# Performance work log

Hardware: AMD Instinct MI355X
Metric: run time of the kernel (lower is better)

Reference implementation:

```python
import jax, jax.numpy as jnp
import numpy as np

BN_EPS = 1e-5
VQ_TEMP = 0.1

B, K, D_AUDIO, D_TEXT, VOCAB = 256, 8, 768, 512, 49408


def setup_inputs() -> dict:
    key = jax.random.key(0)
    k1, k2, k3, k4, k5 = jax.random.split(key, 5)
    return {
        "audio_kw": jax.random.normal(k1, (B, K, D_AUDIO), dtype=jnp.float32),
        "W_proj": jax.random.normal(k2, (D_AUDIO, D_TEXT), dtype=jnp.float32) * 0.02,
        "b_proj": jnp.zeros((D_TEXT,), dtype=jnp.float32),
        "bn_gamma": jax.random.uniform(k3, (D_TEXT,), dtype=jnp.float32, minval=0.5, maxval=1.5),
        "bn_beta": jax.random.normal(k4, (D_TEXT,), dtype=jnp.float32) * 0.01,
        "emb": jax.random.normal(k5, (VOCAB, D_TEXT), dtype=jnp.float32) * 0.02,
    }


def reference(audio_kw, W_proj, b_proj, bn_gamma, bn_beta, emb):
    # keyword projection: [B,K,Da] @ [Da,Dt] -> [B,K,Dt]
    proj = jnp.einsum("bkd,de->bke", audio_kw, W_proj) + b_proj
    # Kw_BatchNorm: batchnorm over (batch, keyword) per text feature, affine
    mean = jnp.mean(proj, axis=(0, 1))
    var = jnp.var(proj, axis=(0, 1))
    bn = (proj - mean) * jax.lax.rsqrt(var + BN_EPS) * bn_gamma + bn_beta
    # cosine similarity against full vocab table (one fused normalize+GEMM,
    # equivalent to the per-keyword F.cosine_similarity loop in the original)
    bn_n = bn / jnp.linalg.norm(bn, axis=-1, keepdims=True)
    emb_n = emb / jnp.linalg.norm(emb, axis=-1, keepdims=True)
    cos_score = jnp.einsum("bke,ve->bkv", bn_n, emb_n)  # [B,K,V]
    # VQ: temperature softmax over the vocab, then soft lookup
    subword_prob = jax.nn.softmax(cos_score / VQ_TEMP, axis=-1)
    vq_keywords = jnp.einsum("bkv,ve->bke", subword_prob, emb)  # [B,K,Dt]
    return vq_keywords
```

## Files before the change

### kernel.cpp

```cpp
#include <hip/hip_runtime.h>
#include <stdint.h>

typedef unsigned short u16;
typedef _Float16 f16;
typedef __attribute__((ext_vector_type(8))) _Float16 f16x8;
typedef __attribute__((ext_vector_type(4))) float f32x4;

#define DA 768
#define DT 512
#define NV 49408
#define MTOT 2048
#define NB_N 193
#define KS 16

__device__ __forceinline__ u16 f2h(float f) {
  return __builtin_bit_cast(u16, (f16)f);
}

__device__ __forceinline__ void gload16(const void* g, void* l) {
  __builtin_amdgcn_global_load_lds((const __attribute__((address_space(1))) void*)g,
                                   (__attribute__((address_space(3))) void*)l,
                                   16, 0, 0);
}
#define SBAR()   __builtin_amdgcn_s_barrier()
#define SCHED0() __builtin_amdgcn_sched_barrier(0)
#define MFMA16(a, b, c) __builtin_amdgcn_mfma_f32_16x16x32_f16((a), (b), (c), 0, 0, 0)

__global__ __launch_bounds__(256) void k_a2h(const float* __restrict__ a,
                                             u16* __restrict__ ah) {
  int i = (blockIdx.x * 256 + threadIdx.x) * 8;
  float4 x = *(const float4*)&a[i];
  float4 y = *(const float4*)&a[i + 4];
  union { u16 u[8]; int4 q; } pk;
  pk.u[0] = f2h(x.x); pk.u[1] = f2h(x.y); pk.u[2] = f2h(x.z); pk.u[3] = f2h(x.w);
  pk.u[4] = f2h(y.x); pk.u[5] = f2h(y.y); pk.u[6] = f2h(y.z); pk.u[7] = f2h(y.w);
  *(int4*)&ah[i] = pk.q;
}

__global__ __launch_bounds__(256) void k_wT(const float* __restrict__ W,
                                            u16* __restrict__ WT) {
  __shared__ float tile[64][65];
  const int k0 = blockIdx.y * 64, n0 = blockIdx.x * 64;
  const int t = threadIdx.x;
  const int r = t >> 4, c4 = (t & 15) * 4;
#pragma unroll
  for (int i = 0; i < 4; ++i) {
    float4 x = *(const float4*)&W[(size_t)(k0 + r + i * 16) * DT + n0 + c4];
    tile[r + i * 16][c4 + 0] = x.x; tile[r + i * 16][c4 + 1] = x.y;
    tile[r + i * 16][c4 + 2] = x.z; tile[r + i * 16][c4 + 3] = x.w;
  }
  __syncthreads();
  const int nr = t >> 2, kc = (t & 3) * 16;
  union { u16 u[8]; int4 q; } p0, p1;
#pragma unroll
  for (int i = 0; i < 8; ++i) p0.u[i] = f2h(tile[kc + i][nr]);
#pragma unroll
  for (int i = 0; i < 8; ++i) p1.u[i] = f2h(tile[kc + 8 + i][nr]);
  u16* dst = WT + (size_t)(n0 + nr) * DA + k0 + kc;
  *(int4*)dst = p0.q;
  *(int4*)(dst + 8) = p1.q;
}

__global__ __launch_bounds__(256) void k_stats(const float* __restrict__ P,
                                               float* __restrict__ pstat) {
  const int t = threadIdx.x;
  const int r0 = blockIdx.x * 32;
  float s0 = 0, q0 = 0, s1 = 0, q1 = 0;
  for (int r = r0; r < r0 + 32; ++r) {
    float x0 = P[(size_t)r * DT + t];
    float x1 = P[(size_t)r * DT + t + 256];
    s0 += x0; q0 += x0 * x0; s1 += x1; q1 += x1 * x1;
  }
  float* d = pstat + (size_t)blockIdx.x * 1024;
  d[t] = s0; d[t + 256] = s1; d[512 + t] = q0; d[768 + t] = q1;
}

__global__ __launch_bounds__(256) void k_stats2(const float* __restrict__ pstat,
                                                float* __restrict__ stats) {
  int c = blockIdx.x * 256 + threadIdx.x;
  float s = 0.f;
  for (int b = 0; b < 64; ++b) s += pstat[(size_t)b * 1024 + c];
  stats[c] = s;
}

__global__ __launch_bounds__(64) void k_bnnorm(const float* __restrict__ P,
                                               const float* __restrict__ stats,
                                               const float* __restrict__ gamma,
                                               const float* __restrict__ beta,
                                               u16* __restrict__ bnn) {
  const int r = blockIdx.x, l = threadIdx.x;
  float v[8];
  float ss = 0.f;
#pragma unroll
  for (int i = 0; i < 8; ++i) {
    int c = l * 8 + i;
    float mean = stats[c] * (1.f / MTOT);
    float var = stats[DT + c] * (1.f / MTOT) - mean * mean;
    float is = rsqrtf(var + 1e-5f);
    float x = (P[(size_t)r * DT + c] - mean) * is * gamma[c] + beta[c];
    v[i] = x; ss += x * x;
  }
#pragma unroll
  for (int off = 32; off > 0; off >>= 1) ss += __shfl_xor(ss, off);
  float rn = rsqrtf(ss);
  union { u16 u[8]; int4 q; } pk;
#pragma unroll
  for (int i = 0; i < 8; ++i) pk.u[i] = f2h(v[i] * rn);
  *(int4*)&bnn[(size_t)r * DT + l * 8] = pk.q;
}

__global__ __launch_bounds__(256) void k_embprep2(const float* __restrict__ emb,
                                                  u16* __restrict__ embH,
                                                  u16* __restrict__ embT,
                                                  float* __restrict__ invn) {
  __shared__ float tile[64][65];
  const int v0 = blockIdx.x * 64;
  const int t = threadIdx.x;
  const int r = t >> 4, c4 = (t & 15) * 4;
  const int vr = t >> 2, hc = (t & 3) * 16;
  const int dr = t >> 2, vc = (t & 3) * 16;
  float ssq = 0.f;
  for (int d0 = 0; d0 < DT; d0 += 64) {
    __syncthreads();
#pragma unroll
    for (int i = 0; i < 4; ++i) {
      float4 x = *(const float4*)&emb[(size_t)(v0 + r + i * 16) * DT + d0 + c4];
      tile[r + i * 16][c4 + 0] = x.x; tile[r + i * 16][c4 + 1] = x.y;
      tile[r + i * 16][c4 + 2] = x.z; tile[r + i * 16][c4 + 3] = x.w;
    }
    __syncthreads();
    union { u16 u[8]; int4 q; } pa, pb;
#pragma unroll
    for (int i = 0; i < 8; ++i) { float f = tile[vr][hc + i];     pa.u[i] = f2h(f); ssq += f * f; }
#pragma unroll
    for (int i = 0; i < 8; ++i) { float f = tile[vr][hc + 8 + i]; pb.u[i] = f2h(f); ssq += f * f; }
    *(int4*)&embH[(size_t)(v0 + vr) * DT + d0 + hc] = pa.q;
    *(int4*)&embH[(size_t)(v0 + vr) * DT + d0 + hc + 8] = pb.q;
    union { u16 u[8]; int4 q; } p0, p1;
#pragma unroll
    for (int i = 0; i < 8; ++i) p0.u[i] = f2h(tile[vc + i][dr]);
#pragma unroll
    for (int i = 0; i < 8; ++i) p1.u[i] = f2h(tile[vc + 8 + i][dr]);
    u16* dst = embT + (size_t)(d0 + dr) * NV + v0 + vc;
    *(int4*)dst = p0.q;
    *(int4*)(dst + 8) = p1.q;
  }
  ssq += __shfl_xor(ssq, 1);
  ssq += __shfl_xor(ssq, 2);
  if ((t & 3) == 0) invn[v0 + vr] = rsqrtf(ssq) * 10.0f;
}

__device__ __forceinline__ void kloop256(const f16* __restrict__ A,
                                         const f16* __restrict__ B,
                                         int lda, int ldb, int NT,
                                         int m0, int n0, int tid,
                                         f16* ldsA, f16* ldsB,
                                         f32x4 (&acc)[4][4]) {
  const int l = tid & 63, lr = l & 15, lg = l >> 4;
  const int w = tid >> 6, wm = w >> 2, wn = w & 3;
  const int rA = tid >> 2, qA = tid & 3;
  const int qsA = qA ^ ((rA >> 1) & 3);
  const f16* gA = A + (size_t)(m0 + rA) * lda + qsA * 8;
  const f16* gB0;
  const f16* gB1;
  { int r = tid >> 2, q = tid & 3; int qs = q ^ ((r >> 1) & 3);
    gB0 = B + (size_t)(n0 + r) * ldb + qs * 8; }
  { int c = tid + 512; int r = c >> 2, q = c & 3; int qs = q ^ ((r >> 1) & 3);
    gB1 = B + (size_t)(n0 + r) * ldb + qs * 8; }
  auto STAGE = [&](int buf, int k0) {
    gload16(gA + k0, (void*)&ldsA[(size_t)buf * 4096 + (size_t)tid * 8]);
    gload16(gB0 + k0, (void*)&ldsB[(size_t)buf * 8192 + (size_t)tid * 8]);
    gload16(gB1 + k0, (void*)&ldsB[(size_t)buf * 8192 + (size_t)(tid + 512) * 8]);
  };
  const int gsw = lg ^ ((lr >> 1) & 3);

  STAGE(0, 0);
  STAGE(1, 32);
  asm volatile("s_waitcnt vmcnt(3)" ::: "memory"); SCHED0();
  SBAR(); SCHED0();
  int cur = 0;
  for (int it = 0; it < NT; ++it) {
    const f16* bufA = ldsA + cur * 4096;
    const f16* bufB = ldsB + cur * 8192;
    f16x8 af[4], bf[4];
#pragma unroll
    for (int i = 0; i < 4; ++i)
      af[i] = *(const f16x8*)&bufA[(wm * 64 + i * 16 + lr) * 32 + gsw * 8];
#pragma unroll
    for (int j = 0; j < 4; ++j)
      bf[j] = *(const f16x8*)&bufB[(wn * 64 + j * 16 + lr) * 32 + gsw * 8];
#pragma unroll
    for (int i = 0; i < 4; ++i)
#pragma unroll
      for (int j = 0; j < 4; ++j)
        acc[i][j] = MFMA16(af[i], bf[j], acc[i][j]);
    asm volatile("s_waitcnt lgkmcnt(0)" ::: "memory"); SCHED0();
    SBAR(); SCHED0();
    if (it + 2 < NT) {
      STAGE(cur, (it + 2) * 32);
      asm volatile("s_waitcnt vmcnt(3)" ::: "memory");
    } else {
      asm volatile("s_waitcnt vmcnt(0)" ::: "memory");
    }
    SCHED0();
    SBAR(); SCHED0();
    cur ^= 1;
  }
}

__global__ __launch_bounds__(512) void k_proj(const f16* __restrict__ A,
                                              const f16* __restrict__ Bt,
                                              const float* __restrict__ bias,
                                              float* __restrict__ P) {
  __shared__ f16 sm[24576];
  const int t = threadIdx.x;
  const int l = t & 63, lr = l & 15, lg = l >> 4;
  const int w = t >> 6, wm = w >> 2, wn = w & 3;
  const int m0 = blockIdx.x * 128;
  const int n0 = blockIdx.y * 256;

  f32x4 acc[4][4];
#pragma unroll
  for (int i = 0; i < 4; ++i)
#pragma unroll
    for (int j = 0; j < 4; ++j) acc[i][j] = (f32x4){0.f, 0.f, 0.f, 0.f};

  kloop256(A, Bt, DA, DA, DA / 32, m0, n0, t, sm, sm + 8192, acc);

#pragma unroll
  for (int j = 0; j < 4; ++j) {
    int col = n0 + wn * 64 + j * 16 + lr;
    float bj = bias[col];
#pragma unroll
    for (int i = 0; i < 4; ++i)
#pragma unroll
      for (int rg = 0; rg < 4; ++rg) {
        int row = m0 + wm * 64 + i * 16 + lg * 4 + rg;
        P[(size_t)row * DT + col] = acc[i][j][rg] + bj;
      }
  }
}

__global__ __launch_bounds__(512) void k_score(const f16* __restrict__ A,
                                               const f16* __restrict__ Bt,
                                               const float* __restrict__ invn,
                                               u16* __restrict__ E,
                                               float* __restrict__ lpart,
                                               int row0, int CH) {
  __shared__ f16 sm[24576];
  __shared__ float psum[512];
  const int t = threadIdx.x;
  const int l = t & 63, lr = l & 15, lg = l >> 4;
  const int w = t >> 6, wm = w >> 2, wn = w & 3;
  const int mB = CH >> 7;
  const int nwg = NB_N * mB;
  const int o = blockIdx.x + blockIdx.y * NB_N;
  const int v = (o & 7) * (nwg >> 3) + (o >> 3);
  const int nb = v / mB, by = v % mB;
  const int n0 = nb * 256;
  const int mloc = by * 128;
  const int m0 = row0 + mloc;

  f32x4 acc[4][4];
#pragma unroll
  for (int i = 0; i < 4; ++i)
#pragma unroll
    for (int j = 0; j < 4; ++j) acc[i][j] = (f32x4){0.f, 0.f, 0.f, 0.f};

  kloop256(A, Bt, DT, DT, DT / 32, m0, n0, t, sm, sm + 8192, acc);

  float inv_j[4];
#pragma unroll
  for (int j = 0; j < 4; ++j) inv_j[j] = invn[n0 + wn * 64 + j * 16 + lr];
  float rs[4][4] = {};
#pragma unroll
  for (int r2 = 0; r2 < 2; ++r2) {
    if (wm == r2) {
#pragma unroll
      for (int i = 0; i < 4; ++i)
#pragma unroll
        for (int j = 0; j < 4; ++j)
#pragma unroll
          for (int rg = 0; rg < 4; ++rg) {
            float e = __expf(acc[i][j][rg] * inv_j[j]);
            rs[i][rg] += e;
            int lrow = i * 16 + lg * 4 + rg;
            sm[lrow * 256 + wn * 64 + j * 16 + lr] = (f16)e;
          }
    }
    __syncthreads();
#pragma unroll
    for (int cc = 0; cc < 4; ++cc) {
      int chunk = t + cc * 512;
      int row = chunk >> 5, g = chunk & 31;
      *(int4*)&E[(size_t)(mloc + r2 * 64 + row) * NV + n0 + g * 8] =
          *(const int4*)&sm[chunk * 8];
    }
    __syncthreads();
  }
#pragma unroll
  for (int m = 1; m <= 8; m <<= 1)
#pragma unroll
    for (int i = 0; i < 4; ++i)
#pragma unroll
      for (int rg = 0; rg < 4; ++rg) rs[i][rg] += __shfl_xor(rs[i][rg], m);
  if (lr == 0) {
#pragma unroll
    for (int i = 0; i < 4; ++i)
#pragma unroll
      for (int rg = 0; rg < 4; ++rg)
        psum[(wm * 64 + i * 16 + lg * 4 + rg) * 4 + wn] = rs[i][rg];
  }
  __syncthreads();
  if (t < 128)
    lpart[(size_t)nb * CH + mloc + t] =
        psum[t * 4 + 0] + psum[t * 4 + 1] + psum[t * 4 + 2] + psum[t * 4 + 3];
}

__global__ __launch_bounds__(512) void k_pv(const f16* __restrict__ A,
                                            const f16* __restrict__ Bt,
                                            float* __restrict__ Op,
                                            int CH) {
  extern __shared__ char lds[];
  f16* ldsA = (f16*)lds;
  f16* ldsB = (f16*)(lds + 16384);
  const int t = threadIdx.x;
  const int l = t & 63, lr = l & 15, lg = l >> 4;
  const int w = t >> 6, wm = w >> 2, wn = w & 3;
  const int mB = CH >> 7;
  const int nwg = mB * KS;
  const int o = blockIdx.x;
  const int v = (o & 7) * (nwg >> 3) + (o >> 3);
  const int m = v % mB, z = v / mB;
  const int m0 = m * 128;
  const int g0 = z * 96 + (z < 8 ? z : 8);
  const int NT = 96 + (z < 8 ? 1 : 0);
  const size_t kb = (size_t)g0 * 32;

  const int rA = t >> 2, qA = t & 3;
  const int qsA = qA ^ ((rA >> 1) & 3);
  const f16* gA = A + (size_t)(m0 + rA) * NV + kb + qsA * 8;
  const f16* gB[4];
#pragma unroll
  for (int s = 0; s < 4; ++s) {
    int c = t + 512 * s;
    int r = c >> 2, q = c & 3;
    int qs = q ^ ((r >> 1) & 3);
    gB[s] = Bt + (size_t)r * NV + kb + qs * 8;
  }
  auto STAGE = [&](int buf, int kt) {
    int k0 = kt * 32;
    gload16(gA + k0, (void*)&ldsA[(size_t)buf * 4096 + (size_t)t * 8]);
    gload16(gB[0] + k0, (void*)&ldsB[(size_t)buf * 16384 + (size_t)t * 8]);
    gload16(gB[1] + k0, (void*)&ldsB[(size_t)buf * 16384 + (size_t)(t + 512) * 8]);
    gload16(gB[2] + k0, (void*)&ldsB[(size_t)buf * 16384 + (size_t)(t + 1024) * 8]);
    gload16(gB[3] + k0, (void*)&ldsB[(size_t)buf * 16384 + (size_t)(t + 1536) * 8]);
  };
  const int gsw = lg ^ ((lr >> 1) & 3);

  f32x4 acc[4][8];
#pragma unroll
  for (int i = 0; i < 4; ++i)
#pragma unroll
    for (int j = 0; j < 8; ++j) acc[i][j] = (f32x4){0.f, 0.f, 0.f, 0.f};

  STAGE(0, 0);
  STAGE(1, 1);
  asm volatile("s_waitcnt vmcnt(5)" ::: "memory"); SCHED0();
  SBAR(); SCHED0();
  int cur = 0;
  for (int it = 0; it < NT; ++it) {
    const f16* bufA = ldsA + cur * 4096;
    const f16* bufB = ldsB + cur * 16384;
    f16x8 af[4], bf[8];
#pragma unroll
    for (int i = 0; i < 4; ++i)
      af[i] = *(const f16x8*)&bufA[(wm * 64 + i * 16 + lr) * 32 + gsw * 8];
#pragma unroll
    for (int j = 0; j < 8; ++j)
      bf[j] = *(const f16x8*)&bufB[(wn * 128 + j * 16 + lr) * 32 + gsw * 8];
#pragma unroll
    for (int i = 0; i < 4; ++i)
#pragma unroll
      for (int j = 0; j < 8; ++j)
        acc[i][j] = MFMA16(af[i], bf[j], acc[i][j]);
    asm volatile("s_waitcnt lgkmcnt(0)" ::: "memory"); SCHED0();
    SBAR(); SCHED0();
    if (it + 2 < NT) {
      STAGE(cur, it + 2);
      asm volatile("s_waitcnt vmcnt(5)" ::: "memory");
    } else {
      asm volatile("s_waitcnt vmcnt(0)" ::: "memory");
    }
    SCHED0();
    SBAR(); SCHED0();
    cur ^= 1;
  }

#pragma unroll
  for (int i = 0; i < 4; ++i)
#pragma unroll
    for (int j = 0; j < 8; ++j)
#pragma unroll
      for (int rg = 0; rg < 4; ++rg) {
        int row = m0 + wm * 64 + i * 16 + lg * 4 + rg;
        int col = wn * 128 + j * 16 + lr;
        Op[((size_t)z * CH + row) * DT + col] = acc[i][j][rg];
      }
}

__global__ __launch_bounds__(256) void k_lred(const float* __restrict__ lp,
                                              float* __restrict__ lv, int CH) {
  int rb = blockIdx.x * 256 + threadIdx.x;
  float s = 0.f;
  for (int nb = 0; nb < NB_N; ++nb) s += lp[(size_t)nb * CH + rb];
  lv[rb] = s;
}

__global__ __launch_bounds__(256) void k_out(const float* __restrict__ Op,
                                             const float* __restrict__ lv,
                                             float* __restrict__ out,
                                             int row0, int CH) {
  int idx = blockIdx.x * 256 + threadIdx.x;
  int rb = idx >> 9, c = idx & 511;
  float s = 0.f;
#pragma unroll
  for (int zz = 0; zz < KS; ++zz) s += Op[((size_t)zz * CH + rb) * DT + c];
  out[(size_t)(row0 + rb) * DT + c] = s / lv[rb];
}

extern "C" void kernel_launch(void* const* d_in, const int* in_sizes, int n_in,
                              void* d_out, int out_size, void* d_ws, size_t ws_size,
                              hipStream_t stream) {
  const float* audio = (const float*)d_in[0];
  const float* W     = (const float*)d_in[1];
  const float* bias  = (const float*)d_in[2];
  const float* gamma = (const float*)d_in[3];
  const float* beta  = (const float*)d_in[4];
  const float* emb   = (const float*)d_in[5];
  float* out = (float*)d_out;

  char* ws = (char*)d_ws;
  size_t off = 0;
  auto alloc = [&](size_t bytes) {
    char* p = ws + off;
    off += (bytes + 255) & ~(size_t)255;
    return p;
  };
  float* proj   = (float*)alloc((size_t)MTOT * DT * 4);
  float* pstat  = (float*)alloc((size_t)64 * 1024 * 4);
  float* stats  = (float*)alloc((size_t)2 * DT * 4);
  u16*   bnnH   = (u16*)alloc((size_t)MTOT * DT * 2);
  u16*   embH   = (u16*)alloc((size_t)NV * DT * 2);
  u16*   embT   = (u16*)alloc((size_t)DT * NV * 2);
  float* invn   = (float*)alloc((size_t)NV * 4);
  u16*   audioH = (u16*)alloc((size_t)MTOT * DA * 2);
  u16*   WT     = (u16*)alloc((size_t)DT * DA * 2);
  size_t fixed_off = off;

  int CH = 2048;
  while (CH > 256) {
    size_t need = fixed_off;
    need += (((size_t)CH * NV * 2) + 255) & ~(size_t)255;
    need += (((size_t)NB_N * CH * 4) + 255) & ~(size_t)255;
    need += (((size_t)CH * 4) + 255) & ~(size_t)255;
    need += (((size_t)KS * CH * DT * 4) + 255) & ~(size_t)255;
    if (need <= ws_size) break;
    CH >>= 1;
  }
  u16*   E     = (u16*)alloc((size_t)CH * NV * 2);
  float* lpart = (float*)alloc((size_t)NB_N * CH * 4);
  float* lvec  = (float*)alloc((size_t)CH * 4);
  float* Op    = (float*)alloc((size_t)KS * CH * DT * 4);
  if (ws_size < off) return;

  hipFuncSetAttribute((const void*)k_pv,
                      hipFuncAttributeMaxDynamicSharedMemorySize, 81920);

  k_a2h<<<dim3(MTOT * DA / 2048), dim3(256), 0, stream>>>(audio, audioH);
  k_wT<<<dim3(DT / 64, DA / 64), dim3(256), 0, stream>>>(W, WT);
  k_proj<<<dim3(MTOT / 128, 2), dim3(512), 0, stream>>>(
      (const f16*)audioH, (const f16*)WT, bias, proj);
  k_stats<<<dim3(64), dim3(256), 0, stream>>>(proj, pstat);
  k_stats2<<<dim3(4), dim3(256), 0, stream>>>(pstat, stats);
  k_bnnorm<<<dim3(MTOT), dim3(64), 0, stream>>>(proj, stats, gamma, beta, bnnH);
  k_embprep2<<<dim3(NV / 64), dim3(256), 0, stream>>>(emb, embH, embT, invn);

  for (int row0 = 0; row0 < MTOT; row0 += CH) {
    k_score<<<dim3(NB_N, CH / 128), dim3(512), 0, stream>>>(
        (const f16*)bnnH, (const f16*)embH, invn, E, lpart, row0, CH);
    k_lred<<<dim3(CH / 256), dim3(256), 0, stream>>>(lpart, lvec, CH);
    k_pv<<<dim3((CH >> 7) * KS), dim3(512), 81920, stream>>>(
        (const f16*)E, (const f16*)embT, Op, CH);
    k_out<<<dim3(CH * 2), dim3(256), 0, stream>>>(Op, lvec, out, row0, CH);
  }
}
```

Baseline: 415.4 us.

## Enlarge score kernel tile to 256x256 with 1024 threads and inline K-loop

The score GEMM workgroup grows from a 128x256 to a 256x256 output tile using 16 waves (1024 threads). It uses a custom double-buffered global_load_lds K-loop with XOR-swizzled LDS and dynamic shared memory, and a remainder-aware XCD block remapping. The larger tile is meant to raise embedding-tile reuse and halve the number of workgroups. The cost is lower occupancy per CU, more LDS per block, and more complex indexing.

```diff
diff --git a/kernel.cpp b/kernel.cpp
--- a/kernel.cpp
+++ b/kernel.cpp
@@ -241,33 +241,81 @@
   }
 }
 
-__global__ __launch_bounds__(512) void k_score(const f16* __restrict__ A,
-                                               const f16* __restrict__ Bt,
-                                               const float* __restrict__ invn,
-                                               u16* __restrict__ E,
-                                               float* __restrict__ lpart,
-                                               int row0, int CH) {
-  __shared__ f16 sm[24576];
-  __shared__ float psum[512];
+__global__ __launch_bounds__(1024) void k_score(const f16* __restrict__ A,
+                                                const f16* __restrict__ Bt,
+                                                const float* __restrict__ invn,
+                                                u16* __restrict__ E,
+                                                float* __restrict__ lpart,
+                                                int row0, int CH) {
+  extern __shared__ char lds[];
+  f16* sm = (f16*)lds;
+  float* psum = (float*)(lds + 65536);
   const int t = threadIdx.x;
   const int l = t & 63, lr = l & 15, lg = l >> 4;
   const int w = t >> 6, wm = w >> 2, wn = w & 3;
-  const int mB = CH >> 7;
+  const int mB = CH >> 8;
   const int nwg = NB_N * mB;
   const int o = blockIdx.x + blockIdx.y * NB_N;
-  const int v = (o & 7) * (nwg >> 3) + (o >> 3);
-  const int nb = v / mB, by = v % mB;
+  const int qd = nwg >> 3, rr = nwg & 7;
+  const int xcd = o & 7, idx = o >> 3;
+  const int v = (xcd < rr ? xcd * (qd + 1) : rr * (qd + 1) + (xcd - rr) * qd) + idx;
+  const int nb = v % NB_N;
+  const int by = v / NB_N;
   const int n0 = nb * 256;
-  const int mloc = by * 128;
+  const int mloc = by * 256;
   const int m0 = row0 + mloc;
 
+  const int rS = t >> 2, qS = t & 3;
+  const int qsS = qS ^ ((rS >> 1) & 3);
+  const f16* gA = A + (size_t)(m0 + rS) * DT + qsS * 8;
+  const f16* gB = Bt + (size_t)(n0 + rS) * DT + qsS * 8;
+  f16* ldsA = &sm[0];
+  f16* ldsB = &sm[16384];
+  auto STAGE = [&](int buf, int k0) {
+    gload16(gA + k0, (void*)&ldsA[(size_t)buf * 8192 + (size_t)t * 8]);
+    gload16(gB + k0, (void*)&ldsB[(size_t)buf * 8192 + (size_t)t * 8]);
+  };
+  const int gsw = lg ^ ((lr >> 1) & 3);
+
   f32x4 acc[4][4];
 #pragma unroll
   for (int i = 0; i < 4; ++i)
 #pragma unroll
     for (int j = 0; j < 4; ++j) acc[i][j] = (f32x4){0.f, 0.f, 0.f, 0.f};
 
-  kloop256(A, Bt, DT, DT, DT / 32, m0, n0, t, sm, sm + 8192, acc);
+  STAGE(0, 0);
+  STAGE(1, 32);
+  asm volatile("s_waitcnt vmcnt(2)" ::: "memory"); SCHED0();
+  SBAR(); SCHED0();
+  int cur = 0;
+  const int nit = DT / 32;
+  for (int it = 0; it < nit; ++it) {
+    const f16* bufA = ldsA + cur * 8192;
+    const f16* bufB = ldsB + cur * 8192;
+    f16x8 af[4], bf[4];
+#pragma unroll
+    for (int i = 0; i < 4; ++i)
+      af[i] = *(const f16x8*)&bufA[(wm * 64 + i * 16 + lr) * 32 + gsw * 8];
+#pragma unroll
+    for (int j = 0; j < 4; ++j)
+      bf[j] = *(const f16x8*)&bufB[(wn * 64 + j * 16 + lr) * 32 + gsw * 8];
+#pragma unroll
+    for (int i = 0; i < 4; ++i)
+#pragma unroll
+      for (int j = 0; j < 4; ++j)
+        acc[i][j] = MFMA16(af[i], bf[j], acc[i][j]);
+    asm volatile("s_waitcnt lgkmcnt(0)" ::: "memory"); SCHED0();
+    SBAR(); SCHED0();
+    if (it + 2 < nit) {
+      STAGE(cur, (it + 2) * 32);
+      asm volatile("s_waitcnt vmcnt(2)" ::: "memory");
+    } else {
+      asm volatile("s_waitcnt vmcnt(0)" ::: "memory");
+    }
+    SCHED0();
+    SBAR(); SCHED0();
+    cur ^= 1;
+  }
 
   float inv_j[4];
 #pragma unroll
@@ -275,7 +323,8 @@
   float rs[4][4] = {};
 #pragma unroll
   for (int r2 = 0; r2 < 2; ++r2) {
-    if (wm == r2) {
+    if ((wm >> 1) == r2) {
+      const int lwm = wm & 1;
 #pragma unroll
       for (int i = 0; i < 4; ++i)
 #pragma unroll
@@ -284,16 +333,16 @@
           for (int rg = 0; rg < 4; ++rg) {
             float e = __expf(acc[i][j][rg] * inv_j[j]);
             rs[i][rg] += e;
-            int lrow = i * 16 + lg * 4 + rg;
+            int lrow = lwm * 64 + i * 16 + lg * 4 + rg;
             sm[lrow * 256 + wn * 64 + j * 16 + lr] = (f16)e;
           }
     }
     __syncthreads();
 #pragma unroll
     for (int cc = 0; cc < 4; ++cc) {
-      int chunk = t + cc * 512;
+      int chunk = t + cc * 1024;
       int row = chunk >> 5, g = chunk & 31;
-      *(int4*)&E[(size_t)(mloc + r2 * 64 + row) * NV + n0 + g * 8] =
+      *(int4*)&E[(size_t)(mloc + r2 * 128 + row) * NV + n0 + g * 8] =
           *(const int4*)&sm[chunk * 8];
     }
     __syncthreads();
@@ -312,7 +361,7 @@
         psum[(wm * 64 + i * 16 + lg * 4 + rg) * 4 + wn] = rs[i][rg];
   }
   __syncthreads();
-  if (t < 128)
+  if (t < 256)
     lpart[(size_t)nb * CH + mloc + t] =
         psum[t * 4 + 0] + psum[t * 4 + 1] + psum[t * 4 + 2] + psum[t * 4 + 3];
 }
@@ -474,6 +523,8 @@
   float* Op    = (float*)alloc((size_t)KS * CH * DT * 4);
   if (ws_size < off) return;
 
+  hipFuncSetAttribute((const void*)k_score,
+                      hipFuncAttributeMaxDynamicSharedMemorySize, 69632);
   hipFuncSetAttribute((const void*)k_pv,
                       hipFuncAttributeMaxDynamicSharedMemorySize, 81920);
 
@@ -487,7 +538,7 @@
   k_embprep2<<<dim3(NV / 64), dim3(256), 0, stream>>>(emb, embH, embT, invn);
 
   for (int row0 = 0; row0 < MTOT; row0 += CH) {
-    k_score<<<dim3(NB_N, CH / 128), dim3(512), 0, stream>>>(
+    k_score<<<dim3(NB_N, CH / 256), dim3(1024), 69632, stream>>>(
         (const f16*)bnnH, (const f16*)embH, invn, E, lpart, row0, CH);
     k_lred<<<dim3(CH / 256), dim3(256), 0, stream>>>(lpart, lvec, CH);
     k_pv<<<dim3((CH >> 7) * KS), dim3(512), 81920, stream>>>(
```

Result: slower. 431.4 us (+3.8%).

## Split PV GEMM into 128x256 tiles via shared kloop and store fp16 partials

Applied to the files above, without the earlier changes.

The PV kernel drops its custom 128x512 tile loop with 80KB of dynamic LDS and reuses the shared 128x256 kloop256 routine with a K offset. The grid gains a factor of two along N, giving smaller per-block register and LDS use and more workgroups for occupancy. The split-K partial sums are now written as fp16 instead of fp32, halving partial-buffer traffic in k_pv and k_out. The cost is that the E tile is loaded twice, once per N half, and the fp16 partials lose precision.

```diff
diff --git a/kernel.cpp b/kernel.cpp
--- a/kernel.cpp
+++ b/kernel.cpp
@@ -15,6 +15,9 @@
 
 __device__ __forceinline__ u16 f2h(float f) {
   return __builtin_bit_cast(u16, (f16)f);
+}
+__device__ __forceinline__ float h2f(u16 u) {
+  return (float)__builtin_bit_cast(f16, u);
 }
 
 __device__ __forceinline__ void gload16(const void* g, void* l) {
@@ -152,7 +155,7 @@
 
 __device__ __forceinline__ void kloop256(const f16* __restrict__ A,
                                          const f16* __restrict__ B,
-                                         int lda, int ldb, int NT,
+                                         int lda, int ldb, size_t kb, int NT,
                                          int m0, int n0, int tid,
                                          f16* ldsA, f16* ldsB,
                                          f32x4 (&acc)[4][4]) {
@@ -160,13 +163,13 @@
   const int w = tid >> 6, wm = w >> 2, wn = w & 3;
   const int rA = tid >> 2, qA = tid & 3;
   const int qsA = qA ^ ((rA >> 1) & 3);
-  const f16* gA = A + (size_t)(m0 + rA) * lda + qsA * 8;
+  const f16* gA = A + (size_t)(m0 + rA) * lda + kb + qsA * 8;
   const f16* gB0;
   const f16* gB1;
   { int r = tid >> 2, q = tid & 3; int qs = q ^ ((r >> 1) & 3);
-    gB0 = B + (size_t)(n0 + r) * ldb + qs * 8; }
+    gB0 = B + (size_t)(n0 + r) * ldb + kb + qs * 8; }
   { int c = tid + 512; int r = c >> 2, q = c & 3; int qs = q ^ ((r >> 1) & 3);
-    gB1 = B + (size_t)(n0 + r) * ldb + qs * 8; }
+    gB1 = B + (size_t)(n0 + r) * ldb + kb + qs * 8; }
   auto STAGE = [&](int buf, int k0) {
     gload16(gA + k0, (void*)&ldsA[(size_t)buf * 4096 + (size_t)tid * 8]);
     gload16(gB0 + k0, (void*)&ldsB[(size_t)buf * 8192 + (size_t)tid * 8]);
@@ -225,7 +228,7 @@
 #pragma unroll
     for (int j = 0; j < 4; ++j) acc[i][j] = (f32x4){0.f, 0.f, 0.f, 0.f};
 
-  kloop256(A, Bt, DA, DA, DA / 32, m0, n0, t, sm, sm + 8192, acc);
+  kloop256(A, Bt, DA, DA, 0, DA / 32, m0, n0, t, sm, sm + 8192, acc);
 
 #pragma unroll
   for (int j = 0; j < 4; ++j) {
@@ -267,7 +270,7 @@
 #pragma unroll
     for (int j = 0; j < 4; ++j) acc[i][j] = (f32x4){0.f, 0.f, 0.f, 0.f};
 
-  kloop256(A, Bt, DT, DT, DT / 32, m0, n0, t, sm, sm + 8192, acc);
+  kloop256(A, Bt, DT, DT, 0, DT / 32, m0, n0, t, sm, sm + 8192, acc);
 
   float inv_j[4];
 #pragma unroll
@@ -319,93 +322,42 @@
 
 __global__ __launch_bounds__(512) void k_pv(const f16* __restrict__ A,
                                             const f16* __restrict__ Bt,
-                                            float* __restrict__ Op,
+                                            u16* __restrict__ Op,
                                             int CH) {
-  extern __shared__ char lds[];
-  f16* ldsA = (f16*)lds;
-  f16* ldsB = (f16*)(lds + 16384);
+  __shared__ f16 sm[24576];
   const int t = threadIdx.x;
   const int l = t & 63, lr = l & 15, lg = l >> 4;
   const int w = t >> 6, wm = w >> 2, wn = w & 3;
   const int mB = CH >> 7;
-  const int nwg = mB * KS;
-  const int o = blockIdx.x;
+  const int nwg = 2 * mB * KS;
+  const int o = blockIdx.x + blockIdx.y * 2 + blockIdx.z * 2 * mB;
   const int v = (o & 7) * (nwg >> 3) + (o >> 3);
-  const int m = v % mB, z = v / mB;
+  const int n = v & 1;
+  const int m = (v >> 1) % mB;
+  const int z = v / (2 * mB);
+  const int n0 = n * 256;
   const int m0 = m * 128;
   const int g0 = z * 96 + (z < 8 ? z : 8);
   const int NT = 96 + (z < 8 ? 1 : 0);
   const size_t kb = (size_t)g0 * 32;
 
-  const int rA = t >> 2, qA = t & 3;
-  const int qsA = qA ^ ((rA >> 1) & 3);
-  const f16* gA = A + (size_t)(m0 + rA) * NV + kb + qsA * 8;
-  const f16* gB[4];
-#pragma unroll
-  for (int s = 0; s < 4; ++s) {
-    int c = t + 512 * s;
-    int r = c >> 2, q = c & 3;
-    int qs = q ^ ((r >> 1) & 3);
-    gB[s] = Bt + (size_t)r * NV + kb + qs * 8;
-  }
-  auto STAGE = [&](int buf, int kt) {
-    int k0 = kt * 32;
-    gload16(gA + k0, (void*)&ldsA[(size_t)buf * 4096 + (size_t)t * 8]);
-    gload16(gB[0] + k0, (void*)&ldsB[(size_t)buf * 16384 + (size_t)t * 8]);
-    gload16(gB[1] + k0, (void*)&ldsB[(size_t)buf * 16384 + (size_t)(t + 512) * 8]);
-    gload16(gB[2] + k0, (void*)&ldsB[(size_t)buf * 16384 + (size_t)(t + 1024) * 8]);
-    gload16(gB[3] + k0, (void*)&ldsB[(size_t)buf * 16384 + (size_t)(t + 1536) * 8]);
-  };
-  const int gsw = lg ^ ((lr >> 1) & 3);
-
-  f32x4 acc[4][8];
+  f32x4 acc[4][4];
 #pragma unroll
   for (int i = 0; i < 4; ++i)
 #pragma unroll
-    for (int j = 0; j < 8; ++j) acc[i][j] = (f32x4){0.f, 0.f, 0.f, 0.f};
-
-  STAGE(0, 0);
-  STAGE(1, 1);
-  asm volatile("s_waitcnt vmcnt(5)" ::: "memory"); SCHED0();
-  SBAR(); SCHED0();
-  int cur = 0;
-  for (int it = 0; it < NT; ++it) {
-    const f16* bufA = ldsA + cur * 4096;
-    const f16* bufB = ldsB + cur * 16384;
-    f16x8 af[4], bf[8];
-#pragma unroll
-    for (int i = 0; i < 4; ++i)
-      af[i] = *(const f16x8*)&bufA[(wm * 64 + i * 16 + lr) * 32 + gsw * 8];
-#pragma unroll
-    for (int j = 0; j < 8; ++j)
-      bf[j] = *(const f16x8*)&bufB[(wn * 128 + j * 16 + lr) * 32 + gsw * 8];
-#pragma unroll
-    for (int i = 0; i < 4; ++i)
-#pragma unroll
-      for (int j = 0; j < 8; ++j)
-        acc[i][j] = MFMA16(af[i], bf[j], acc[i][j]);
-    asm volatile("s_waitcnt lgkmcnt(0)" ::: "memory"); SCHED0();
-    SBAR(); SCHED0();
-    if (it + 2 < NT) {
-      STAGE(cur, it + 2);
-      asm volatile("s_waitcnt vmcnt(5)" ::: "memory");
-    } else {
-      asm volatile("s_waitcnt vmcnt(0)" ::: "memory");
-    }
-    SCHED0();
-    SBAR(); SCHED0();
-    cur ^= 1;
-  }
+    for (int j = 0; j < 4; ++j) acc[i][j] = (f32x4){0.f, 0.f, 0.f, 0.f};
+
+  kloop256(A, Bt, NV, NV, kb, NT, m0, n0, t, sm, sm + 8192, acc);
 
 #pragma unroll
   for (int i = 0; i < 4; ++i)
 #pragma unroll
-    for (int j = 0; j < 8; ++j)
+    for (int j = 0; j < 4; ++j)
 #pragma unroll
       for (int rg = 0; rg < 4; ++rg) {
         int row = m0 + wm * 64 + i * 16 + lg * 4 + rg;
-        int col = wn * 128 + j * 16 + lr;
-        Op[((size_t)z * CH + row) * DT + col] = acc[i][j][rg];
+        int col = n0 + wn * 64 + j * 16 + lr;
+        Op[((size_t)z * CH + row) * DT + col] = f2h(acc[i][j][rg]);
       }
 }
 
@@ -417,7 +369,7 @@
   lv[rb] = s;
 }
 
-__global__ __launch_bounds__(256) void k_out(const float* __restrict__ Op,
+__global__ __launch_bounds__(256) void k_out(const u16* __restrict__ Op,
                                              const float* __restrict__ lv,
                                              float* __restrict__ out,
                                              int row0, int CH) {
@@ -425,7 +377,7 @@
   int rb = idx >> 9, c = idx & 511;
   float s = 0.f;
 #pragma unroll
-  for (int zz = 0; zz < KS; ++zz) s += Op[((size_t)zz * CH + rb) * DT + c];
+  for (int zz = 0; zz < KS; ++zz) s += h2f(Op[((size_t)zz * CH + rb) * DT + c]);
   out[(size_t)(row0 + rb) * DT + c] = s / lv[rb];
 }
 
@@ -464,18 +416,15 @@
     need += (((size_t)CH * NV * 2) + 255) & ~(size_t)255;
     need += (((size_t)NB_N * CH * 4) + 255) & ~(size_t)255;
     need += (((size_t)CH * 4) + 255) & ~(size_t)255;
-    need += (((size_t)KS * CH * DT * 4) + 255) & ~(size_t)255;
+    need += (((size_t)KS * CH * DT * 2) + 255) & ~(size_t)255;
     if (need <= ws_size) break;
     CH >>= 1;
   }
   u16*   E     = (u16*)alloc((size_t)CH * NV * 2);
   float* lpart = (float*)alloc((size_t)NB_N * CH * 4);
   float* lvec  = (float*)alloc((size_t)CH * 4);
-  float* Op    = (float*)alloc((size_t)KS * CH * DT * 4);
+  u16*   Op    = (u16*)alloc((size_t)KS * CH * DT * 2);
   if (ws_size < off) return;
-
-  hipFuncSetAttribute((const void*)k_pv,
-                      hipFuncAttributeMaxDynamicSharedMemorySize, 81920);
 
   k_a2h<<<dim3(MTOT * DA / 2048), dim3(256), 0, stream>>>(audio, audioH);
   k_wT<<<dim3(DT / 64, DA / 64), dim3(256), 0, stream>>>(W, WT);
@@ -490,7 +439,7 @@
     k_score<<<dim3(NB_N, CH / 128), dim3(512), 0, stream>>>(
         (const f16*)bnnH, (const f16*)embH, invn, E, lpart, row0, CH);
     k_lred<<<dim3(CH / 256), dim3(256), 0, stream>>>(lpart, lvec, CH);
-    k_pv<<<dim3((CH >> 7) * KS), dim3(512), 81920, stream>>>(
+    k_pv<<<dim3(2, CH / 128, KS), dim3(512), 0, stream>>>(
         (const f16*)E, (const f16*)embT, Op, CH);
     k_out<<<dim3(CH * 2), dim3(256), 0, stream>>>(Op, lvec, out, row0, CH);
   }
```

Result: faster. 402.5 us (-3.1%).
